# Kernel optimization log

Hardware: AMD Instinct MI355X
Metric: run time of the kernel (lower is better)

## Reference

```python
import jax, jax.numpy as jnp
import numpy as np

IN_FEATURES = 4096
OUT_FEATURES = 4096
RANK = 16
N_BITS = 4
SCALING = 0.01
QMIN = -(2 ** (N_BITS - 1))      # -8
QMAX = 2 ** (N_BITS - 1) - 1     #  7
EPS = 1e-8


@jax.custom_vjp
def ste_quant(x, scale):
    """Fake-quantize with straight-through estimator (zero_point = 0)."""
    q = jnp.clip(jnp.round(x / scale), QMIN, QMAX)
    return q * scale


def _ste_fwd(x, scale):
    return ste_quant(x, scale), (x, scale)


def _ste_bwd(res, g):
    x, scale = res
    q = x / scale
    mask = ((q >= QMIN) & (q <= QMAX)).astype(g.dtype)
    # Torch STE returns grad only for input; scale gets no gradient.
    gs = jnp.zeros(scale.shape, dtype=g.dtype)
    return (g * mask, gs)


ste_quant.defvjp(_ste_fwd, _ste_bwd)


def setup_inputs() -> dict:
    key = jax.random.key(0)
    ks = jax.random.split(key, 4)
    x = jax.random.normal(ks[0], (4, 2048, IN_FEATURES), dtype=jnp.float32)
    pretrained_weight = 0.1 * jax.random.normal(ks[1], (OUT_FEATURES, IN_FEATURES), dtype=jnp.float32)
    lora_A = np.sqrt(2.0 / RANK) * jax.random.normal(ks[2], (RANK, IN_FEATURES), dtype=jnp.float32)
    # Original inits lora_B to zeros; use small random values so the LoRA path is non-degenerate.
    lora_B = 0.01 * jax.random.normal(ks[3], (OUT_FEATURES, RANK), dtype=jnp.float32)
    # Mirror initialize_scales(): per-channel 99th-percentile |w| / 2^(n_bits-1).
    weight_max = jnp.quantile(jnp.abs(pretrained_weight), 0.99, axis=1)
    weight_scale = weight_max / (2 ** (N_BITS - 1))
    activation_scale = jnp.ones((1,), dtype=jnp.float32)
    bias = jnp.zeros((OUT_FEATURES,), dtype=jnp.float32)
    return {
        "x": x,
        "pretrained_weight": pretrained_weight,
        "lora_A": lora_A,
        "lora_B": lora_B,
        "weight_scale": weight_scale,
        "activation_scale": activation_scale,
        "bias": bias,
    }


def reference(x, pretrained_weight, lora_A, lora_B, weight_scale, activation_scale, bias):
    # LoRA merge: [out, in]
    merged = pretrained_weight + SCALING * (lora_B @ lora_A)
    wsc = jnp.maximum(jnp.abs(weight_scale), EPS)      # [out]
    asc = jnp.maximum(jnp.abs(activation_scale), EPS)  # [1]
    # Per-output-channel fake quant of the weight (vectorized over the torch loop).
    w_q = ste_quant(merged, wsc[:, None])              # [out, in]
    x_q = ste_quant(x, asc)                            # [b, s, in]
    # F.linear: x_q @ w_q^T + bias
    return jnp.einsum("bsi,oi->bso", x_q, w_q) + bias
```

## Files before the change

### kernel.cpp

```cpp
#include <hip/hip_runtime.h>
#include <cstdint>
#include <cstddef>

#define IN_F 4096
#define OUT_F 4096
#define RANKK 16
#define EPSQ 1e-8f
#define LSCALE 0.01f

typedef __attribute__((ext_vector_type(4))) int i32x4;
typedef __attribute__((ext_vector_type(16))) int i32x16;

__device__ __forceinline__ float quantf(float v, float s) {
    float q = rintf(v / s);
    return fminf(7.f, fmaxf(-8.f, q));
}

__global__ __launch_bounds__(256) void qx_kernel(const float* __restrict__ x,
                                                 const float* __restrict__ ascale,
                                                 int8_t* __restrict__ qx) {
    const float asc = fmaxf(fabsf(ascale[0]), EPSQ);
    const int i = blockIdx.x * 256 + threadIdx.x;
    float4 v = ((const float4*)x)[i];
    union { int8_t b[4]; int w; } u;
    u.b[0] = (int8_t)(int)quantf(v.x, asc);
    u.b[1] = (int8_t)(int)quantf(v.y, asc);
    u.b[2] = (int8_t)(int)quantf(v.z, asc);
    u.b[3] = (int8_t)(int)quantf(v.w, asc);
    ((int*)qx)[i] = u.w;
}

__global__ __launch_bounds__(256) void qw_kernel(const float* __restrict__ W,
                                                 const float* __restrict__ lA,
                                                 const float* __restrict__ lB,
                                                 const float* __restrict__ wscale,
                                                 int8_t* __restrict__ qw) {
    __shared__ float Ablk[RANKK][256];
    __shared__ float Bblk[64][RANKK];
    const int tid = threadIdx.x;
    const int i0 = blockIdx.x * 256;
    const int o0 = blockIdx.y * 64;

#pragma unroll
    for (int r = 0; r < RANKK; ++r)
        Ablk[r][tid] = lA[r * IN_F + i0 + tid];
    for (int j = tid; j < 64 * RANKK; j += 256)
        Bblk[j >> 4][j & 15] = lB[(size_t)(o0 + (j >> 4)) * RANKK + (j & 15)];
    __syncthreads();

    const int i = i0 + tid;
#pragma unroll 4
    for (int o = 0; o < 64; ++o) {
        float s = 0.f;
#pragma unroll
        for (int r = 0; r < RANKK; ++r) s += Bblk[o][r] * Ablk[r][tid];
        float merged = W[(size_t)(o0 + o) * IN_F + i] + LSCALE * s;
        float wsc = fmaxf(fabsf(wscale[o0 + o]), EPSQ);
        qw[(size_t)(o0 + o) * IN_F + i] = (int8_t)(int)quantf(merged, wsc);
    }
}

constexpr int BM = 128, BN = 256, BK = 128, KD = 4096;

__global__ __launch_bounds__(256, 2) void gemm_i8_kernel(
        const int8_t* __restrict__ qx, const int8_t* __restrict__ qw,
        const float* __restrict__ wscale, const float* __restrict__ ascale,
        const float* __restrict__ bias, float* __restrict__ out) {
    __shared__ __attribute__((aligned(16))) int8_t As[BM * BK];
    __shared__ __attribute__((aligned(16))) int8_t Bs[BN * BK];

    const int tid  = threadIdx.x;
    const int lane = tid & 63;
    const int wave = tid >> 6;
    const int hi   = lane >> 5;
    const int m_tile = blockIdx.y * BM;
    const int n_tile = blockIdx.x * BN;
    const int wm = (wave >> 1) * 64;
    const int wn = (wave & 1) * 128;

    int srcA[4], srcB[8];
#pragma unroll
    for (int is = 0; is < 4; ++is) {
        int p = is * 256 + tid;
        int m = p >> 3;
        int q = (p & 7) ^ (m & 7);
        srcA[is] = m * KD + q * 16;
    }
#pragma unroll
    for (int is = 0; is < 8; ++is) {
        int p = is * 256 + tid;
        int m = p >> 3;
        int q = (p & 7) ^ (m & 7);
        srcB[is] = m * KD + q * 16;
    }
    const int8_t* Abase = qx + (size_t)m_tile * KD;
    const int8_t* Bbase = qw + (size_t)n_tile * KD;

    int baseA[2], maskA[2], baseB[4], maskB[4];
#pragma unroll
    for (int mi = 0; mi < 2; ++mi) {
        const int ra = wm + mi * 32 + (lane & 31);
        baseA[mi] = ra * BK;
        maskA[mi] = ra & 7;
    }
#pragma unroll
    for (int ni = 0; ni < 4; ++ni) {
        const int rb = wn + ni * 32 + (lane & 31);
        baseB[ni] = rb * BK;
        maskB[ni] = rb & 7;
    }

    i32x16 acc[2][4];
#pragma unroll
    for (int mi = 0; mi < 2; ++mi)
#pragma unroll
        for (int ni = 0; ni < 4; ++ni) acc[mi][ni] = (i32x16)(0);

    for (int k0 = 0; k0 < KD; k0 += BK) {
#pragma unroll
        for (int is = 0; is < 4; ++is)
            __builtin_amdgcn_global_load_lds(
                (const __attribute__((address_space(1))) void*)(Abase + k0 + srcA[is]),
                (__attribute__((address_space(3))) void*)(As + (is * 256 + wave * 64) * 16),
                16, 0, 0);
#pragma unroll
        for (int is = 0; is < 8; ++is)
            __builtin_amdgcn_global_load_lds(
                (const __attribute__((address_space(1))) void*)(Bbase + k0 + srcB[is]),
                (__attribute__((address_space(3))) void*)(Bs + (is * 256 + wave * 64) * 16),
                16, 0, 0);
        __syncthreads();
#pragma unroll
        for (int kk = 0; kk < 4; ++kk) {
            const int q = kk * 2 + hi;
            i32x4 af[2], bf[4];
#pragma unroll
            for (int mi = 0; mi < 2; ++mi)
                af[mi] = *(const i32x4*)(As + baseA[mi] + ((q ^ maskA[mi]) * 16));
#pragma unroll
            for (int ni = 0; ni < 4; ++ni)
                bf[ni] = *(const i32x4*)(Bs + baseB[ni] + ((q ^ maskB[ni]) * 16));
#pragma unroll
            for (int mi = 0; mi < 2; ++mi)
#pragma unroll
                for (int ni = 0; ni < 4; ++ni)
                    acc[mi][ni] = __builtin_amdgcn_mfma_i32_32x32x32_i8(
                        af[mi], bf[ni], acc[mi][ni], 0, 0, 0);
        }
        __syncthreads();
    }

    const float asc = fmaxf(fabsf(ascale[0]), EPSQ);
#pragma unroll
    for (int ni = 0; ni < 4; ++ni) {
        const int n  = n_tile + wn + ni * 32 + (lane & 31);
        const float sc = asc * fmaxf(fabsf(wscale[n]), EPSQ);
        const float bb = bias[n];
#pragma unroll
        for (int mi = 0; mi < 2; ++mi) {
            const int rbase = m_tile + wm + mi * 32 + 4 * hi;
#pragma unroll
            for (int r = 0; r < 16; ++r) {
                const int row = rbase + (r & 3) + 8 * (r >> 2);
                out[(size_t)row * OUT_F + n] = sc * (float)acc[mi][ni][r] + bb;
            }
        }
    }
}

extern "C" void kernel_launch(void* const* d_in, const int* in_sizes, int n_in,
                              void* d_out, int out_size, void* d_ws, size_t ws_size,
                              hipStream_t stream) {
    const float* x      = (const float*)d_in[0];
    const float* W      = (const float*)d_in[1];
    const float* lA     = (const float*)d_in[2];
    const float* lB     = (const float*)d_in[3];
    const float* wscale = (const float*)d_in[4];
    const float* ascale = (const float*)d_in[5];
    const float* bias   = (const float*)d_in[6];
    float* out = (float*)d_out;

    const int M = in_sizes[0] / IN_F;
    int8_t* qx = (int8_t*)d_ws;
    int8_t* qw = qx + (size_t)M * IN_F;

    qx_kernel<<<(in_sizes[0] / 4 + 255) / 256, 256, 0, stream>>>(x, ascale, qx);
    qw_kernel<<<dim3(IN_F / 256, OUT_F / 64), 256, 0, stream>>>(W, lA, lB, wscale, qw);
    gemm_i8_kernel<<<dim3(OUT_F / BN, M / BM), 256, 0, stream>>>(
        qx, qw, wscale, ascale, bias, out);
}
```

Measured before the change: 419.5 us.

## Restructure int8 GEMM with 256x256 tiles, double-buffered LDS and interleaved prefetch

```diff
diff --git a/kernel.cpp b/kernel.cpp
--- a/kernel.cpp
+++ b/kernel.cpp
@@ -60,104 +60,156 @@
     }
 }
 
-constexpr int BM = 128, BN = 256, BK = 128, KD = 4096;
-
-__global__ __launch_bounds__(256, 2) void gemm_i8_kernel(
+constexpr int BM = 256, BN = 256, BK = 128, KD = 4096, NT = KD / BK;
+
+__device__ __forceinline__ void gll16(const int8_t* g, int8_t* l) {
+    __builtin_amdgcn_global_load_lds(
+        (const __attribute__((address_space(1))) void*)g,
+        (__attribute__((address_space(3))) void*)l, 16, 0, 0);
+}
+
+#define LOAD_AF(MB)                                                           \
+    { _Pragma("unroll") for (int i_ = 0; i_ < 2; ++i_) {                      \
+        _Pragma("unroll") for (int ks_ = 0; ks_ < 4; ++ks_)                   \
+            af[i_][ks_] = *(const i32x4*)(Asb + aB[(MB) + i_] +               \
+                                          ((ks_ ^ aH[(MB) + i_]) << 5));      \
+    } }
+
+#define LOAD_BF(NI)                                                           \
+    { _Pragma("unroll") for (int ks_ = 0; ks_ < 4; ++ks_)                     \
+        bf[ks_] = *(const i32x4*)(Bsb + bB[(NI)] + ((ks_ ^ bH[(NI)]) << 5)); }
+
+#define MMA8(MB, NI)                                                          \
+    { __builtin_amdgcn_s_setprio(1);                                          \
+      _Pragma("unroll") for (int ks_ = 0; ks_ < 4; ++ks_) {                   \
+          acc[(MB)][(NI)] = __builtin_amdgcn_mfma_i32_32x32x32_i8(            \
+              af[0][ks_], bf[ks_], acc[(MB)][(NI)], 0, 0, 0);                 \
+          acc[(MB) + 1][(NI)] = __builtin_amdgcn_mfma_i32_32x32x32_i8(        \
+              af[1][ks_], bf[ks_], acc[(MB) + 1][(NI)], 0, 0, 0);             \
+      }                                                                       \
+      __builtin_amdgcn_s_setprio(0); }
+
+__global__ __launch_bounds__(512, 2) void gemm_i8_kernel(
         const int8_t* __restrict__ qx, const int8_t* __restrict__ qw,
         const float* __restrict__ wscale, const float* __restrict__ ascale,
         const float* __restrict__ bias, float* __restrict__ out) {
-    __shared__ __attribute__((aligned(16))) int8_t As[BM * BK];
-    __shared__ __attribute__((aligned(16))) int8_t Bs[BN * BK];
+    __shared__ __attribute__((aligned(16))) int8_t As[2][BM * BK];
+    __shared__ __attribute__((aligned(16))) int8_t Bs[2][BN * BK];
 
     const int tid  = threadIdx.x;
     const int lane = tid & 63;
     const int wave = tid >> 6;
     const int hi   = lane >> 5;
-    const int m_tile = blockIdx.y * BM;
-    const int n_tile = blockIdx.x * BN;
-    const int wm = (wave >> 1) * 64;
-    const int wn = (wave & 1) * 128;
-
-    int srcA[4], srcB[8];
-#pragma unroll
-    for (int is = 0; is < 4; ++is) {
-        int p = is * 256 + tid;
-        int m = p >> 3;
-        int q = (p & 7) ^ (m & 7);
-        srcA[is] = m * KD + q * 16;
-    }
-#pragma unroll
-    for (int is = 0; is < 8; ++is) {
-        int p = is * 256 + tid;
-        int m = p >> 3;
-        int q = (p & 7) ^ (m & 7);
-        srcB[is] = m * KD + q * 16;
-    }
-    const int8_t* Abase = qx + (size_t)m_tile * KD;
-    const int8_t* Bbase = qw + (size_t)n_tile * KD;
-
-    int baseA[2], maskA[2], baseB[4], maskB[4];
-#pragma unroll
-    for (int mi = 0; mi < 2; ++mi) {
-        const int ra = wm + mi * 32 + (lane & 31);
-        baseA[mi] = ra * BK;
-        maskA[mi] = ra & 7;
-    }
-#pragma unroll
-    for (int ni = 0; ni < 4; ++ni) {
-        const int rb = wn + ni * 32 + (lane & 31);
-        baseB[ni] = rb * BK;
-        maskB[ni] = rb & 7;
-    }
-
-    i32x16 acc[2][4];
-#pragma unroll
-    for (int mi = 0; mi < 2; ++mi)
-#pragma unroll
-        for (int ni = 0; ni < 4; ++ni) acc[mi][ni] = (i32x16)(0);
-
-    for (int k0 = 0; k0 < KD; k0 += BK) {
-#pragma unroll
-        for (int is = 0; is < 4; ++is)
-            __builtin_amdgcn_global_load_lds(
-                (const __attribute__((address_space(1))) void*)(Abase + k0 + srcA[is]),
-                (__attribute__((address_space(3))) void*)(As + (is * 256 + wave * 64) * 16),
-                16, 0, 0);
-#pragma unroll
-        for (int is = 0; is < 8; ++is)
-            __builtin_amdgcn_global_load_lds(
-                (const __attribute__((address_space(1))) void*)(Bbase + k0 + srcB[is]),
-                (__attribute__((address_space(3))) void*)(Bs + (is * 256 + wave * 64) * 16),
-                16, 0, 0);
-        __syncthreads();
-#pragma unroll
-        for (int kk = 0; kk < 4; ++kk) {
-            const int q = kk * 2 + hi;
-            i32x4 af[2], bf[4];
-#pragma unroll
-            for (int mi = 0; mi < 2; ++mi)
-                af[mi] = *(const i32x4*)(As + baseA[mi] + ((q ^ maskA[mi]) * 16));
-#pragma unroll
-            for (int ni = 0; ni < 4; ++ni)
-                bf[ni] = *(const i32x4*)(Bs + baseB[ni] + ((q ^ maskB[ni]) * 16));
-#pragma unroll
-            for (int mi = 0; mi < 2; ++mi)
-#pragma unroll
-                for (int ni = 0; ni < 4; ++ni)
-                    acc[mi][ni] = __builtin_amdgcn_mfma_i32_32x32x32_i8(
-                        af[mi], bf[ni], acc[mi][ni], 0, 0, 0);
-        }
-        __syncthreads();
+
+    const int bid  = blockIdx.x;
+    const int swz  = (bid & 7) * 64 + (bid >> 3);
+    const int m_tile = (swz >> 4) * BM;
+    const int n_tile = (swz & 15) * BN;
+
+    const int wm = (wave >> 2) * 128;
+    const int wn = (wave & 3) * 64;
+
+    int off[2];
+#pragma unroll
+    for (int j = 0; j < 2; ++j) {
+        int pc = j * 512 + tid;
+        int r  = pc >> 3;
+        off[j] = r * KD + (((pc & 7) ^ (r & 7)) << 4);
+    }
+    const int lds_u = wave * 1024;
+
+    int aB[4], aH[4];
+#pragma unroll
+    for (int mi = 0; mi < 4; ++mi) {
+        int row = wm + mi * 32 + (lane & 31);
+        aB[mi] = row * BK + ((hi ^ (row & 1)) << 4);
+        aH[mi] = (row >> 1) & 3;
+    }
+    int bB[2], bH[2];
+#pragma unroll
+    for (int ni = 0; ni < 2; ++ni) {
+        int row = wn + ni * 32 + (lane & 31);
+        bB[ni] = row * BK + ((hi ^ (row & 1)) << 4);
+        bH[ni] = (row >> 1) & 3;
+    }
+
+    const int8_t* Ab = qx + (size_t)m_tile * KD;
+    const int8_t* Bb = qw + (size_t)n_tile * KD;
+
+    i32x16 acc[4][2];
+#pragma unroll
+    for (int mi = 0; mi < 4; ++mi)
+#pragma unroll
+        for (int ni = 0; ni < 2; ++ni) acc[mi][ni] = (i32x16)(0);
+
+#pragma unroll
+    for (int h = 0; h < 2; ++h)
+#pragma unroll
+        for (int j = 0; j < 2; ++j)
+            gll16(Ab + h * 128 * KD + off[j],
+                  &As[0][h * 16384 + j * 8192 + lds_u]);
+#pragma unroll
+    for (int h = 0; h < 2; ++h)
+#pragma unroll
+        for (int j = 0; j < 2; ++j)
+            gll16(Bb + h * 128 * KD + off[j],
+                  &Bs[0][h * 16384 + j * 8192 + lds_u]);
+
+    i32x4 af[2][4], bf[4];
+
+    for (int t = 0; t < NT - 1; ++t) {
+        const int buf = t & 1, nb = buf ^ 1;
+        const int8_t* Asb = As[buf];
+        const int8_t* Bsb = Bs[buf];
+        const int8_t* Ag  = Ab + (t + 1) * BK;
+        const int8_t* Bg  = Bb + (t + 1) * BK;
+
+        gll16(Ag + off[0], &As[nb][lds_u]);
+        gll16(Ag + off[1], &As[nb][8192 + lds_u]);
+        asm volatile("s_waitcnt vmcnt(2)" ::: "memory");
+        __builtin_amdgcn_s_barrier();
+        LOAD_AF(0); LOAD_BF(0);
+        MMA8(0, 0);
+        __builtin_amdgcn_s_barrier();
+
+        LOAD_BF(1);
+        gll16(Ag + 128 * KD + off[0], &As[nb][16384 + lds_u]);
+        gll16(Ag + 128 * KD + off[1], &As[nb][16384 + 8192 + lds_u]);
+        MMA8(0, 1);
+        __builtin_amdgcn_s_barrier();
+
+        LOAD_AF(2); LOAD_BF(0);
+        gll16(Bg + off[0], &Bs[nb][lds_u]);
+        gll16(Bg + off[1], &Bs[nb][8192 + lds_u]);
+        MMA8(2, 0);
+        __builtin_amdgcn_s_barrier();
+
+        LOAD_BF(1);
+        gll16(Bg + 128 * KD + off[0], &Bs[nb][16384 + lds_u]);
+        gll16(Bg + 128 * KD + off[1], &Bs[nb][16384 + 8192 + lds_u]);
+        MMA8(2, 1);
+        __builtin_amdgcn_s_barrier();
+    }
+
+    {
+        const int8_t* Asb = As[(NT - 1) & 1];
+        const int8_t* Bsb = Bs[(NT - 1) & 1];
+        asm volatile("s_waitcnt vmcnt(0)" ::: "memory");
+        __builtin_amdgcn_s_barrier();
+        LOAD_AF(0); LOAD_BF(0); MMA8(0, 0);
+        LOAD_BF(1);             MMA8(0, 1);
+        LOAD_AF(2); LOAD_BF(0); MMA8(2, 0);
+        LOAD_BF(1);             MMA8(2, 1);
     }
 
     const float asc = fmaxf(fabsf(ascale[0]), EPSQ);
 #pragma unroll
-    for (int ni = 0; ni < 4; ++ni) {
+    for (int ni = 0; ni < 2; ++ni) {
         const int n  = n_tile + wn + ni * 32 + (lane & 31);
         const float sc = asc * fmaxf(fabsf(wscale[n]), EPSQ);
         const float bb = bias[n];
 #pragma unroll
-        for (int mi = 0; mi < 2; ++mi) {
+        for (int mi = 0; mi < 4; ++mi) {
             const int rbase = m_tile + wm + mi * 32 + 4 * hi;
 #pragma unroll
             for (int r = 0; r < 16; ++r) {
@@ -186,6 +238,6 @@
 
     qx_kernel<<<(in_sizes[0] / 4 + 255) / 256, 256, 0, stream>>>(x, ascale, qx);
     qw_kernel<<<dim3(IN_F / 256, OUT_F / 64), 256, 0, stream>>>(W, lA, lB, wscale, qw);
-    gemm_i8_kernel<<<dim3(OUT_F / BN, M / BM), 256, 0, stream>>>(
+    gemm_i8_kernel<<<dim3((M / BM) * (OUT_F / BN)), 512, 0, stream>>>(
         qx, qw, wscale, ascale, bias, out);
 }
```

Measured after the change: 454.2 us. 8.3% more time.

## Double-buffer int8 GEMM LDS tiles, enlarge block tile, swizzle block order

Applied to the files above, without the earlier changes.

```diff
diff --git a/kernel.cpp b/kernel.cpp
--- a/kernel.cpp
+++ b/kernel.cpp
@@ -60,55 +60,59 @@
     }
 }
 
-constexpr int BM = 128, BN = 256, BK = 128, KD = 4096;
-
-__global__ __launch_bounds__(256, 2) void gemm_i8_kernel(
+constexpr int BM = 256, BN = 256, BK = 128, KD = 4096, NT = KD / BK;
+
+__device__ __forceinline__ void gll16(const int8_t* g, const int8_t* l) {
+    __builtin_amdgcn_global_load_lds(
+        (const __attribute__((address_space(1))) void*)g,
+        (__attribute__((address_space(3))) void*)l, 16, 0, 0);
+}
+
+__global__ __launch_bounds__(512, 2) void gemm_i8_kernel(
         const int8_t* __restrict__ qx, const int8_t* __restrict__ qw,
         const float* __restrict__ wscale, const float* __restrict__ ascale,
         const float* __restrict__ bias, float* __restrict__ out) {
-    __shared__ __attribute__((aligned(16))) int8_t As[BM * BK];
-    __shared__ __attribute__((aligned(16))) int8_t Bs[BN * BK];
+    __shared__ __attribute__((aligned(16))) int8_t As[2][BM * BK];
+    __shared__ __attribute__((aligned(16))) int8_t Bs[2][BN * BK];
 
     const int tid  = threadIdx.x;
     const int lane = tid & 63;
     const int wave = tid >> 6;
     const int hi   = lane >> 5;
-    const int m_tile = blockIdx.y * BM;
-    const int n_tile = blockIdx.x * BN;
+
+    const int bid  = blockIdx.x;
+    const int swz  = (bid & 7) * 64 + (bid >> 3);
+    const int m_tile = (swz >> 4) * BM;
+    const int n_tile = (swz & 15) * BN;
+
     const int wm = (wave >> 1) * 64;
     const int wn = (wave & 1) * 128;
 
-    int srcA[4], srcB[8];
+    int src[4];
 #pragma unroll
     for (int is = 0; is < 4; ++is) {
-        int p = is * 256 + tid;
+        int p = is * 512 + tid;
         int m = p >> 3;
-        int q = (p & 7) ^ (m & 7);
-        srcA[is] = m * KD + q * 16;
-    }
-#pragma unroll
-    for (int is = 0; is < 8; ++is) {
-        int p = is * 256 + tid;
-        int m = p >> 3;
-        int q = (p & 7) ^ (m & 7);
-        srcB[is] = m * KD + q * 16;
-    }
-    const int8_t* Abase = qx + (size_t)m_tile * KD;
-    const int8_t* Bbase = qw + (size_t)n_tile * KD;
-
-    int baseA[2], maskA[2], baseB[4], maskB[4];
+        src[is] = m * KD + (((p & 7) ^ (m & 7)) << 4);
+    }
+    const int lds_u = wave * 1024;
+
+    int aB[2], aH[2], bB[4], bH[4];
 #pragma unroll
     for (int mi = 0; mi < 2; ++mi) {
         const int ra = wm + mi * 32 + (lane & 31);
-        baseA[mi] = ra * BK;
-        maskA[mi] = ra & 7;
+        aB[mi] = ra * BK;
+        aH[mi] = ra & 7;
     }
 #pragma unroll
     for (int ni = 0; ni < 4; ++ni) {
         const int rb = wn + ni * 32 + (lane & 31);
-        baseB[ni] = rb * BK;
-        maskB[ni] = rb & 7;
-    }
+        bB[ni] = rb * BK;
+        bH[ni] = rb & 7;
+    }
+
+    const int8_t* Ab = qx + (size_t)m_tile * KD;
+    const int8_t* Bb = qw + (size_t)n_tile * KD;
 
     i32x16 acc[2][4];
 #pragma unroll
@@ -116,30 +120,39 @@
 #pragma unroll
         for (int ni = 0; ni < 4; ++ni) acc[mi][ni] = (i32x16)(0);
 
-    for (int k0 = 0; k0 < KD; k0 += BK) {
-#pragma unroll
-        for (int is = 0; is < 4; ++is)
-            __builtin_amdgcn_global_load_lds(
-                (const __attribute__((address_space(1))) void*)(Abase + k0 + srcA[is]),
-                (__attribute__((address_space(3))) void*)(As + (is * 256 + wave * 64) * 16),
-                16, 0, 0);
-#pragma unroll
-        for (int is = 0; is < 8; ++is)
-            __builtin_amdgcn_global_load_lds(
-                (const __attribute__((address_space(1))) void*)(Bbase + k0 + srcB[is]),
-                (__attribute__((address_space(3))) void*)(Bs + (is * 256 + wave * 64) * 16),
-                16, 0, 0);
-        __syncthreads();
+#pragma unroll
+    for (int is = 0; is < 4; ++is)
+        gll16(Ab + src[is], &As[0][is * 8192 + lds_u]);
+#pragma unroll
+    for (int is = 0; is < 4; ++is)
+        gll16(Bb + src[is], &Bs[0][is * 8192 + lds_u]);
+    __syncthreads();
+
+    for (int t = 0; t < NT; ++t) {
+        const int buf = t & 1;
+        if (t + 1 < NT) {
+            const int k1 = (t + 1) * BK;
+            int8_t* dA = (int8_t*)As[buf ^ 1];
+            int8_t* dB = (int8_t*)Bs[buf ^ 1];
+#pragma unroll
+            for (int is = 0; is < 4; ++is)
+                gll16(Ab + k1 + src[is], dA + is * 8192 + lds_u);
+#pragma unroll
+            for (int is = 0; is < 4; ++is)
+                gll16(Bb + k1 + src[is], dB + is * 8192 + lds_u);
+        }
+        const int8_t* Asb = As[buf];
+        const int8_t* Bsb = Bs[buf];
 #pragma unroll
         for (int kk = 0; kk < 4; ++kk) {
             const int q = kk * 2 + hi;
             i32x4 af[2], bf[4];
 #pragma unroll
             for (int mi = 0; mi < 2; ++mi)
-                af[mi] = *(const i32x4*)(As + baseA[mi] + ((q ^ maskA[mi]) * 16));
+                af[mi] = *(const i32x4*)(Asb + aB[mi] + ((q ^ aH[mi]) << 4));
 #pragma unroll
             for (int ni = 0; ni < 4; ++ni)
-                bf[ni] = *(const i32x4*)(Bs + baseB[ni] + ((q ^ maskB[ni]) * 16));
+                bf[ni] = *(const i32x4*)(Bsb + bB[ni] + ((q ^ bH[ni]) << 4));
 #pragma unroll
             for (int mi = 0; mi < 2; ++mi)
 #pragma unroll
@@ -147,7 +160,7 @@
                     acc[mi][ni] = __builtin_amdgcn_mfma_i32_32x32x32_i8(
                         af[mi], bf[ni], acc[mi][ni], 0, 0, 0);
         }
-        __syncthreads();
+        if (t + 1 < NT) __syncthreads();
     }
 
     const float asc = fmaxf(fabsf(ascale[0]), EPSQ);
@@ -186,6 +199,6 @@
 
     qx_kernel<<<(in_sizes[0] / 4 + 255) / 256, 256, 0, stream>>>(x, ascale, qx);
     qw_kernel<<<dim3(IN_F / 256, OUT_F / 64), 256, 0, stream>>>(W, lA, lB, wscale, qw);
-    gemm_i8_kernel<<<dim3(OUT_F / BN, M / BM), 256, 0, stream>>>(
+    gemm_i8_kernel<<<dim3((M / BM) * (OUT_F / BN)), 512, 0, stream>>>(
         qx, qw, wscale, ascale, bias, out);
 }
```

Measured after the change: 437.7 us. 1.04x slower.
